# Optimization experiments

Hardware: AMD Instinct MI355X
Metric: run time of the kernel (lower is better)

The kernel has to match this reference:

```python
import jax, jax.numpy as jnp
import numpy as np

B = 8192      # graphs per batch
NPG = 40      # nodes per graph (= average_nodes, uniform here)
DEG = 16      # avg degree
IN = 64
HID = 32
OUT = 10
K1 = 20       # ceil(0.5*40)
K2 = 10       # ceil(0.5*20)
N = B * NPG
E = N * DEG
EPS = 1e-15


def _lin_params(k, fi, fo):
    kw, kb = jax.random.split(k)
    s = 1.0 / np.sqrt(fi)
    w = jax.random.uniform(kw, (fi, fo), jnp.float32, -s, s)
    b = jax.random.uniform(kb, (fo,), jnp.float32, -s, s)
    return w, b


def setup_inputs():
    key = jax.random.key(0)
    ks = jax.random.split(key, 14)
    x = jax.random.normal(ks[0], (N, IN), jnp.float32)
    # edges constrained within each graph (graphs are contiguous blocks of NPG nodes)
    g = jnp.repeat(jnp.arange(B, dtype=jnp.int32), NPG * DEG)
    src = g * NPG + jax.random.randint(ks[1], (E,), 0, NPG, dtype=jnp.int32)
    dst = g * NPG + jax.random.randint(ks[2], (E,), 0, NPG, dtype=jnp.int32)
    edge_index = jnp.stack([src, dst])
    batch = jnp.repeat(jnp.arange(B, dtype=jnp.int32), NPG)
    w_c1, b_c1 = _lin_params(ks[3], IN, HID)
    w_p1, b_p1 = _lin_params(ks[4], HID, K1)
    w2r, b2 = _lin_params(ks[5], HID, HID)
    w2o, _ = _lin_params(ks[6], HID, HID)
    w_p2, b_p2 = _lin_params(ks[7], HID, K2)
    w3r, b3 = _lin_params(ks[8], HID, HID)
    w3o, _ = _lin_params(ks[9], HID, HID)
    w_l1, b_l1 = _lin_params(ks[10], HID, HID)
    w_l2, b_l2 = _lin_params(ks[11], HID, OUT)
    return dict(x=x, edge_index=edge_index, batch=batch,
                w_c1=w_c1, b_c1=b_c1, w_p1=w_p1, b_p1=b_p1,
                w2r=w2r, b2=b2, w2o=w2o, w_p2=w_p2, b_p2=b_p2,
                w3r=w3r, b3=b3, w3o=w3o,
                w_l1=w_l1, b_l1=b_l1, w_l2=w_l2, b_l2=b_l2)


def _gcn_conv(x, edge_index, w, b):
    # PyG GCNConv: x' = D^-1/2 (A + I) D^-1/2 (X W) + b, unit edge weights
    h = x @ w
    row, col = edge_index
    deg = jnp.zeros((N,), h.dtype).at[col].add(1.0) + 1.0  # +1 self loop
    dinv = jax.lax.rsqrt(deg)
    msg = (dinv[row] * dinv[col])[:, None] * h[row]
    out = jnp.zeros_like(h).at[col].add(msg)
    out = out + (dinv * dinv)[:, None] * h  # self-loop contribution
    return out + b


def _dense_mincut_pool(x, adj, s, mask=None):
    # faithful to torch_geometric.nn.dense_mincut_pool
    s = jax.nn.softmax(s, axis=-1)
    if mask is not None:
        m = mask[..., None].astype(x.dtype)
        x = x * m
        s = s * m
    k = s.shape[-1]
    out = jnp.einsum('bnk,bnf->bkf', s, x)
    out_adj = jnp.einsum('bnk,bnm,bml->bkl', s, adj, s)
    mincut_num = jnp.trace(out_adj, axis1=1, axis2=2)
    d_flat = adj.sum(-1)                                   # [B, n]
    mincut_den = jnp.einsum('bnk,bn,bnk->b', s, d_flat, s)  # tr(S^T D S)
    mincut_loss = jnp.mean(-(mincut_num / mincut_den))
    ss = jnp.einsum('bnk,bnl->bkl', s, s)
    ss_norm = jnp.sqrt(jnp.sum(ss * ss, axis=(1, 2), keepdims=True))
    i_s = jnp.eye(k, dtype=x.dtype) / jnp.sqrt(jnp.asarray(k, x.dtype))
    ortho_loss = jnp.mean(jnp.sqrt(jnp.sum((ss / ss_norm - i_s) ** 2, axis=(1, 2))))
    # zero diagonal, then symmetric degree-normalize coarse adjacency
    eye = jnp.eye(k, dtype=x.dtype)
    out_adj = out_adj * (1.0 - eye)
    d = jnp.sqrt(out_adj.sum(-1))[:, None, :] + EPS        # [B,1,k]
    out_adj = out_adj / d / jnp.swapaxes(d, 1, 2)
    return out, out_adj, mincut_loss, ortho_loss


def _dense_graph_conv(x, adj, w_rel, b, w_root):
    # PyG DenseGraphConv (aggr='add'): lin_rel(A @ x) + lin_root(x); lin_root bias=False
    return (adj @ x) @ w_rel + b + x @ w_root


def reference(x, edge_index, batch, w_c1, b_c1, w_p1, b_p1, w2r, b2, w2o,
              w_p2, b_p2, w3r, b3, w3o, w_l1, b_l1, w_l2, b_l2):
    h = jax.nn.relu(_gcn_conv(x, edge_index, w_c1, b_c1))
    # to_dense_batch (uniform NPG nodes per graph, batch sorted)
    local = jnp.arange(N, dtype=jnp.int32) - batch * NPG
    xd = jnp.zeros((B, NPG, HID), h.dtype).at[batch, local].set(h)
    mask = jnp.ones((B, NPG), bool)
    # to_dense_adj (accumulates duplicate edges)
    row, col = edge_index
    g = batch[row]
    adj = jnp.zeros((B, NPG, NPG), h.dtype).at[g, row - g * NPG, col - g * NPG].add(1.0)
    s = xd @ w_p1 + b_p1
    xd, adj, mc1, o1 = _dense_mincut_pool(xd, adj, s, mask)
    xd = jax.nn.relu(_dense_graph_conv(xd, adj, w2r, b2, w2o))
    s = xd @ w_p2 + b_p2
    xd, adj, mc2, o2 = _dense_mincut_pool(xd, adj, s)
    xd = _dense_graph_conv(xd, adj, w3r, b3, w3o)
    pooled = xd.mean(axis=1)
    out = jax.nn.relu(pooled @ w_l1 + b_l1) @ w_l2 + b_l2
    return out, mc1 + mc2 + o1 + o2
```

## Files before the change

### kernel.cpp

```cpp
#include <hip/hip_runtime.h>

#define NT 256

constexpr int Bg   = 8192;
constexpr int NPG  = 40;
constexpr int EPG  = 640;
constexpr int IN_  = 64;
constexpr int HID  = 32;
constexpr int K1   = 20;
constexpr int K2   = 10;
constexpr int OUTC = 10;
constexpr int NE   = Bg * NPG * 16;
constexpr int SH   = 36;
constexpr float EPSF = 1e-15f;

#define FMA4(acc, a, b) do { \
    float _s = (a); \
    acc.x = fmaf(_s, (b).x, acc.x); \
    acc.y = fmaf(_s, (b).y, acc.y); \
    acc.z = fmaf(_s, (b).z, acc.z); \
    acc.w = fmaf(_s, (b).w, acc.w); } while (0)

__device__ __forceinline__ float wave_red(float v) {
#pragma unroll
    for (int off = 32; off > 0; off >>= 1) v += __shfl_down(v, off, 64);
    return v;
}

__global__ __launch_bounds__(NT, 4)
void mincut_fused(const float* __restrict__ x, const int* __restrict__ ei,
                  const float* __restrict__ w_c1, const float* __restrict__ b_c1,
                  const float* __restrict__ w_p1, const float* __restrict__ b_p1,
                  const float* __restrict__ w2r_, const float* __restrict__ b2_,
                  const float* __restrict__ w2o_,
                  const float* __restrict__ w_p2, const float* __restrict__ b_p2,
                  const float* __restrict__ w3r_, const float* __restrict__ b3_,
                  const float* __restrict__ w3o_,
                  const float* __restrict__ w_l1, const float* __restrict__ b_l1,
                  const float* __restrict__ w_l2, const float* __restrict__ b_l2,
                  float* __restrict__ out, float* __restrict__ wsg)
{
    __shared__ __align__(16) float sA_[NPG * NPG];
    __shared__ __align__(16) float bufH[NPG * SH];
    __shared__ __align__(16) float bufXd[NPG * SH];
    __shared__ __align__(16) float bufS[NPG * K1];
    __shared__ __align__(16) float bufAS[NPG * K1];
    __shared__ __align__(16) float sSS[K1 * K1];
    __shared__ __align__(16) float sdinv[NPG];
    __shared__ __align__(16) float srowsA[NPG];
    __shared__ __align__(16) float srowm[NPG];
    __shared__ __align__(16) float sden[NPG];
    __shared__ __align__(16) float sred1[2];
    __shared__ __align__(16) float sred2[2];
    __shared__ __align__(16) float sc[8];

    float* sA2  = sA_;
    float* sX2  = bufH;
    float* sW2r = bufH + 720;
    float* sW2o = bufAS;
    float* sS2  = bufS;
    float* sAS2 = bufS + 200;
    float* sA3  = bufS + 400;
    float* sSS2 = bufS + 500;
    float* sW3r = bufXd;
    float* sW3o = bufXd + 360;
    float* sX3  = bufXd + 720;
    float* sX4  = bufXd + 1080;

    const int g    = blockIdx.x;
    const int tid  = threadIdx.x;
    const int lane = tid & 63;
    const int wid  = tid >> 6;

    int er0, ec0, er1, ec1, er2 = -1, ec2 = 0;
    {
        const int eb = g * EPG, nb = g * NPG;
        const int* srcp = ei;
        const int* dstp = ei + NE;
        int e = eb + tid;
        er0 = srcp[e] - nb; ec0 = dstp[e] - nb;
        e += NT;
        er1 = srcp[e] - nb; ec1 = dstp[e] - nb;
        if (tid + 2 * NT < EPG) {
            e += NT;
            er2 = srcp[e] - nb; ec2 = dstp[e] - nb;
        }
    }
    for (int i = tid; i < NPG * NPG; i += NT) sA_[i] = 0.f;
    __syncthreads();

    atomicAdd(&sA_[er0 * NPG + ec0], 1.f);
    atomicAdd(&sA_[er1 * NPG + ec1], 1.f);
    if (er2 >= 0) atomicAdd(&sA_[er2 * NPG + ec2], 1.f);

    if (tid < 160) {
        int np = tid >> 3, fq = tid & 7;
        int n0 = 2 * np, n1 = n0 + 1;
        const float4* x0 = (const float4*)(x + (size_t)g * (NPG * IN_) + n0 * IN_);
        const float4* x1 = (const float4*)(x + (size_t)g * (NPG * IN_) + n1 * IN_);
        const float4* wg = (const float4*)w_c1;
        float4 acc0 = {0.f,0.f,0.f,0.f}, acc1 = {0.f,0.f,0.f,0.f};
#pragma unroll 4
        for (int kk = 0; kk < IN_ / 4; kk++) {
            float4 a0 = x0[kk], a1 = x1[kk];
            float4 w0 = wg[(4*kk+0)*8 + fq];
            float4 w1 = wg[(4*kk+1)*8 + fq];
            float4 w2 = wg[(4*kk+2)*8 + fq];
            float4 w3 = wg[(4*kk+3)*8 + fq];
            FMA4(acc0, a0.x, w0); FMA4(acc0, a0.y, w1);
            FMA4(acc0, a0.z, w2); FMA4(acc0, a0.w, w3);
            FMA4(acc1, a1.x, w0); FMA4(acc1, a1.y, w1);
            FMA4(acc1, a1.z, w2); FMA4(acc1, a1.w, w3);
        }
        ((float4*)(bufH + n0 * SH))[fq] = acc0;
        ((float4*)(bufH + n1 * SH))[fq] = acc1;
    }
    __syncthreads();

    if (tid < NPG) {
        float s = 0.f;
#pragma unroll
        for (int r = 0; r < NPG; r++) s += sA_[r * NPG + tid];
        sdinv[tid] = rsqrtf(s + 1.f);
    } else if (tid >= 64 && tid < 64 + NPG) {
        int n = tid - 64; float s = 0.f;
#pragma unroll
        for (int m = 0; m < NPG; m++) s += sA_[n * NPG + m];
        srowsA[n] = s;
    }
    __syncthreads();

    if (tid < 160) {
        int cp = tid >> 3, fq = tid & 7;
        int c0 = 2 * cp, c1 = c0 + 1;
        float4 acc0 = {0.f,0.f,0.f,0.f}, acc1 = {0.f,0.f,0.f,0.f};
#pragma unroll 8
        for (int r = 0; r < NPG; r++) {
            float2 a2 = *(const float2*)&sA_[r * NPG + c0];
            float dv = sdinv[r];
            float4 b = ((const float4*)(bufH + r * SH))[fq];
            FMA4(acc0, a2.x * dv, b);
            FMA4(acc1, a2.y * dv, b);
        }
        float4 bb = ((const float4*)b_c1)[fq];
        float4 h0 = ((const float4*)(bufH + c0 * SH))[fq];
        float4 h1 = ((const float4*)(bufH + c1 * SH))[fq];
        float d0 = sdinv[c0], d1 = sdinv[c1];
        float4 r0, r1;
        r0.x = fmaxf(fmaf(d0, fmaf(d0, h0.x, acc0.x), bb.x), 0.f);
        r0.y = fmaxf(fmaf(d0, fmaf(d0, h0.y, acc0.y), bb.y), 0.f);
        r0.z = fmaxf(fmaf(d0, fmaf(d0, h0.z, acc0.z), bb.z), 0.f);
        r0.w = fmaxf(fmaf(d0, fmaf(d0, h0.w, acc0.w), bb.w), 0.f);
        r1.x = fmaxf(fmaf(d1, fmaf(d1, h1.x, acc1.x), bb.x), 0.f);
        r1.y = fmaxf(fmaf(d1, fmaf(d1, h1.y, acc1.y), bb.y), 0.f);
        r1.z = fmaxf(fmaf(d1, fmaf(d1, h1.z, acc1.z), bb.z), 0.f);
        r1.w = fmaxf(fmaf(d1, fmaf(d1, h1.w, acc1.w), bb.w), 0.f);
        ((float4*)(bufXd + c0 * SH))[fq] = r0;
        ((float4*)(bufXd + c1 * SH))[fq] = r1;
    }
    __syncthreads();

    if (tid < 100) {
        int np = tid / 5, lq = tid - np * 5;
        int n0 = 2 * np, n1 = n0 + 1;
        const float4* wg = (const float4*)w_p1;
        float4 bb = ((const float4*)b_p1)[lq];
        float4 acc0 = bb, acc1 = bb;
#pragma unroll 8
        for (int k = 0; k < HID; k++) {
            float a0 = bufXd[n0 * SH + k];
            float a1 = bufXd[n1 * SH + k];
            float4 w = wg[k * 5 + lq];
            FMA4(acc0, a0, w);
            FMA4(acc1, a1, w);
        }
        ((float4*)(bufS + n0 * K1))[lq] = acc0;
        ((float4*)(bufS + n1 * K1))[lq] = acc1;
    }
    __syncthreads();

    if (tid < NPG) {
        float* row = bufS + tid * K1;
        float v[K1]; float m = -3.0e38f;
#pragma unroll
        for (int k = 0; k < K1; k++) { v[k] = row[k]; m = fmaxf(m, v[k]); }
        float ssum = 0.f;
#pragma unroll
        for (int k = 0; k < K1; k++) { v[k] = __expf(v[k] - m); ssum += v[k]; }
        float inv = 1.f / ssum;
#pragma unroll
        for (int k = 0; k < K1; k++) row[k] = v[k] * inv;
    }
    __syncthreads();

    if (tid < 100) {
        int np = tid / 5, lq = tid - np * 5;
        int n0 = 2 * np, n1 = n0 + 1;
        const float4* sb = (const float4*)bufS;
        float4 acc0 = {0.f,0.f,0.f,0.f}, acc1 = {0.f,0.f,0.f,0.f};
#pragma unroll
        for (int m4 = 0; m4 < NPG / 4; m4++) {
            float4 a0 = *(const float4*)&sA_[n0 * NPG + 4 * m4];
            float4 a1 = *(const float4*)&sA_[n1 * NPG + 4 * m4];
            float4 b0 = sb[(4*m4+0)*5 + lq];
            float4 b1 = sb[(4*m4+1)*5 + lq];
            float4 b2v = sb[(4*m4+2)*5 + lq];
            float4 b3v = sb[(4*m4+3)*5 + lq];
            FMA4(acc0, a0.x, b0); FMA4(acc0, a0.y, b1);
            FMA4(acc0, a0.z, b2v); FMA4(acc0, a0.w, b3v);
            FMA4(acc1, a1.x, b0); FMA4(acc1, a1.y, b1);
            FMA4(acc1, a1.z, b2v); FMA4(acc1, a1.w, b3v);
        }
        ((float4*)(bufAS + n0 * K1))[lq] = acc0;
        ((float4*)(bufAS + n1 * K1))[lq] = acc1;
    } else if (tid < 150) {
        int oo = tid - 100;
        int kp = oo / 5, lq = oo - kp * 5;
        int k0 = 2 * kp, k1 = k0 + 1;
        float4 acc0 = {0.f,0.f,0.f,0.f}, acc1 = {0.f,0.f,0.f,0.f};
#pragma unroll 8
        for (int n = 0; n < NPG; n++) {
            float2 s2v = *(const float2*)&bufS[n * K1 + k0];
            float4 b = ((const float4*)(bufS + n * K1))[lq];
            FMA4(acc0, s2v.x, b);
            FMA4(acc1, s2v.y, b);
        }
        ((float4*)(sSS + k0 * K1))[lq] = acc0;
        ((float4*)(sSS + k1 * K1))[lq] = acc1;
    }
    __syncthreads();

    if (tid < 50) {
        int kp = tid / 5, lq = tid - kp * 5;
        int k0 = 2 * kp, k1 = k0 + 1;
        float4 acc0 = {0.f,0.f,0.f,0.f}, acc1 = {0.f,0.f,0.f,0.f};
#pragma unroll 8
        for (int n = 0; n < NPG; n++) {
            float2 s2v = *(const float2*)&bufS[n * K1 + k0];
            float4 b = ((const float4*)(bufAS + n * K1))[lq];
            FMA4(acc0, s2v.x, b);
            FMA4(acc1, s2v.y, b);
        }
        ((float4*)(sA2 + k0 * K1))[lq] = acc0;
        ((float4*)(sA2 + k1 * K1))[lq] = acc1;
    } else if (tid < 130) {
        int oo = tid - 50;
        int kp = oo >> 3, fq = oo & 7;
        int k0 = 2 * kp, k1 = k0 + 1;
        float4 acc0 = {0.f,0.f,0.f,0.f}, acc1 = {0.f,0.f,0.f,0.f};
#pragma unroll 8
        for (int n = 0; n < NPG; n++) {
            float2 s2v = *(const float2*)&bufS[n * K1 + k0];
            float4 b = ((const float4*)(bufXd + n * SH))[fq];
            FMA4(acc0, s2v.x, b);
            FMA4(acc1, s2v.y, b);
        }
        ((float4*)(sX2 + k0 * SH))[fq] = acc0;
        ((float4*)(sX2 + k1 * SH))[fq] = acc1;
    } else if (tid < 170) {
        int n = tid - 130;
        float s2 = 0.f;
#pragma unroll
        for (int k = 0; k < K1; k++) { float v = bufS[n * K1 + k]; s2 = fmaf(v, v, s2); }
        sden[n] = srowsA[n] * s2;
    } else if (wid == 3) {
        float v = 0.f;
        for (int i = lane; i < K1 * K1; i += 64) { float t = sSS[i]; v = fmaf(t, t, v); }
        v = wave_red(v); if (lane == 0) sc[2] = v;
    }
    __syncthreads();

    if (wid < 2) {
        float rn = 1.f / sqrtf(sc[2]);
        const float isk = 0.22360679774997896f;
        float p = 0.f;
        for (int o = tid; o < K1 * K1; o += 128) {
            int k = o / K1, l = o - k * K1;
            float v = sSS[o] * rn - ((k == l) ? isk : 0.f);
            p = fmaf(v, v, p);
        }
        p = wave_red(p);
        if (lane == 0) sred1[wid] = p;
    } else if (wid == 2) {
        float v = (lane < K1) ? sA2[lane * (K1 + 1)] : 0.f;
        v = wave_red(v); if (lane == 0) sc[0] = v;
        if (lane < K1) {
            float s = 0.f;
#pragma unroll
            for (int l = 0; l < K1; l++) s += sA2[lane * K1 + l];
            s -= sA2[lane * (K1 + 1)];
            srowm[lane] = 1.f / (sqrtf(s) + EPSF);
        }
    } else {
        float v = (lane < NPG) ? sden[lane] : 0.f;
        v = wave_red(v); if (lane == 0) sc[1] = v;
    }
    for (int o = tid; o < 320; o += NT) {
        bool first = (o < 160);
        int oo = first ? o : o - 160;
        int n = oo >> 3, fq = oo & 7;
        const float4* wg = (const float4*)(first ? w2r_ : w2o_);
        float4 acc = {0.f,0.f,0.f,0.f};
#pragma unroll 8
        for (int k = 0; k < HID; k++) {
            float a = sX2[n * SH + k];
            FMA4(acc, a, wg[k * 8 + fq]);
        }
        if (first) ((float4*)(sW2r + n * SH))[fq] = acc;
        else       ((float4*)(sW2o + n * SH))[fq] = acc;
    }
    __syncthreads();

    if (tid < 80) {
        int kp = tid >> 3, fq = tid & 7;
        int k0 = 2 * kp, k1 = k0 + 1;
        float4 acc0 = {0.f,0.f,0.f,0.f}, acc1 = {0.f,0.f,0.f,0.f};
#pragma unroll
        for (int l = 0; l < K1; l++) {
            float rl = srowm[l];
            float a0 = (l == k0) ? 0.f : sA2[k0 * K1 + l];
            float a1 = (l == k1) ? 0.f : sA2[k1 * K1 + l];
            float4 w = ((const float4*)(sW2r + l * SH))[fq];
            FMA4(acc0, a0 * rl, w);
            FMA4(acc1, a1 * rl, w);
        }
        float4 bb = ((const float4*)b2_)[fq];
        float4 o0 = ((const float4*)(sW2o + k0 * SH))[fq];
        float4 o1 = ((const float4*)(sW2o + k1 * SH))[fq];
        float rk0 = srowm[k0], rk1 = srowm[k1];
        float4 r0, r1;
        r0.x = fmaxf(fmaf(rk0, acc0.x, o0.x + bb.x), 0.f);
        r0.y = fmaxf(fmaf(rk0, acc0.y, o0.y + bb.y), 0.f);
        r0.z = fmaxf(fmaf(rk0, acc0.z, o0.z + bb.z), 0.f);
        r0.w = fmaxf(fmaf(rk0, acc0.w, o0.w + bb.w), 0.f);
        r1.x = fmaxf(fmaf(rk1, acc1.x, o1.x + bb.x), 0.f);
        r1.y = fmaxf(fmaf(rk1, acc1.y, o1.y + bb.y), 0.f);
        r1.z = fmaxf(fmaf(rk1, acc1.z, o1.z + bb.z), 0.f);
        r1.w = fmaxf(fmaf(rk1, acc1.w, o1.w + bb.w), 0.f);
        ((float4*)(sX2 + k0 * SH))[fq] = r0;
        ((float4*)(sX2 + k1 * SH))[fq] = r1;
    }
    __syncthreads();

    if (tid < K1 * K2) {
        int n = tid / K2, q = tid - n * K2;
        float acc = b_p2[q];
#pragma unroll 8
        for (int j = 0; j < HID; j++) acc = fmaf(sX2[n * SH + j], w_p2[j * K2 + q], acc);
        sS2[tid] = acc;
    }
    __syncthreads();

    if (tid < K1) {
        float* row = sS2 + tid * K2;
        float v[K2]; float m = -3.0e38f;
#pragma unroll
        for (int q = 0; q < K2; q++) { v[q] = row[q]; m = fmaxf(m, v[q]); }
        float ssum = 0.f;
#pragma unroll
        for (int q = 0; q < K2; q++) { v[q] = __expf(v[q] - m); ssum += v[q]; }
        float inv = 1.f / ssum;
#pragma unroll
        for (int q = 0; q < K2; q++) row[q] = v[q] * inv;
    }
    __syncthreads();

    for (int o = tid; o < 400; o += NT) {
        if (o < 200) {
            int n = o / K2, l = o - n * K2;
            float acc = 0.f;
#pragma unroll
            for (int m = 0; m < K1; m++) {
                float a = (m == n) ? 0.f : sA2[n * K1 + m];
                acc = fmaf(a * srowm[m], sS2[m * K2 + l], acc);
            }
            sAS2[n * K2 + l] = acc * srowm[n];
        } else if (o < 300) {
            int oo = o - 200; int k = oo / K2, l = oo - k * K2;
            float acc = 0.f;
#pragma unroll
            for (int n = 0; n < K1; n++) acc = fmaf(sS2[n * K2 + k], sS2[n * K2 + l], acc);
            sSS2[k * K2 + l] = acc;
        } else if (o < 380) {
            int oo = o - 300; int k = oo >> 3, fq = oo & 7;
            float4 acc = {0.f, 0.f, 0.f, 0.f};
#pragma unroll
            for (int n = 0; n < K1; n++) {
                float a = sS2[n * K2 + k];
                float4 b = ((const float4*)(sX2 + n * SH))[fq];
                FMA4(acc, a, b);
            }
            ((float4*)(sX3 + k * SH))[fq] = acc;
        } else {
            int n = o - 380;
            float da = 0.f, s2 = 0.f;
#pragma unroll
            for (int l = 0; l < K1; l++) {
                float a = (l == n) ? 0.f : sA2[n * K1 + l];
                da = fmaf(a, srowm[l], da);
            }
            da *= srowm[n];
#pragma unroll
            for (int q = 0; q < K2; q++) { float v = sS2[n * K2 + q]; s2 = fmaf(v, v, s2); }
            sden[n] = da * s2;
        }
    }
    __syncthreads();

    if (tid < K2 * K2) {
        int k = tid / K2, l = tid - k * K2;
        float acc = 0.f;
#pragma unroll
        for (int n = 0; n < K1; n++) acc = fmaf(sS2[n * K2 + k], sAS2[n * K2 + l], acc);
        sA3[tid] = acc;
    } else if (wid == 2) {
        float v = (lane < K1) ? sden[lane] : 0.f;
        v = wave_red(v); if (lane == 0) sc[5] = v;
    } else if (wid == 3) {
        float v = 0.f;
        for (int i = lane; i < K2 * K2; i += 64) { float t = sSS2[i]; v = fmaf(t, t, v); }
        v = wave_red(v); if (lane == 0) sc[6] = v;
    }
    __syncthreads();

    if (wid == 0) {
        float rn = 1.f / sqrtf(sc[6]);
        const float isk = 0.31622776601683794f;
        float p = 0.f;
        for (int i = lane; i < K2 * K2; i += 64) {
            int k = i / K2, l = i - k * K2;
            float v = sSS2[i] * rn - ((k == l) ? isk : 0.f);
            p = fmaf(v, v, p);
        }
        p = wave_red(p);
        if (lane == 0) sred2[0] = p;
    } else if (wid == 1) {
        float v = (lane < K2) ? sA3[lane * (K2 + 1)] : 0.f;
        v = wave_red(v); if (lane == 0) sc[4] = v;
        if (lane < K2) {
            float s = 0.f;
#pragma unroll
            for (int l = 0; l < K2; l++) s += sA3[lane * K2 + l];
            s -= sA3[lane * (K2 + 1)];
            srowm[lane] = 1.f / (sqrtf(s) + EPSF);
        }
    }
    __syncthreads();

    if (tid < 160) {
        bool first = (tid < 80);
        int oo = first ? tid : tid - 80;
        int n = oo >> 3, fq = oo & 7;
        const float4* wg = (const float4*)(first ? w3r_ : w3o_);
        float4 acc = {0.f,0.f,0.f,0.f};
#pragma unroll 8
        for (int k = 0; k < HID; k++) {
            float a = sX3[n * SH + k];
            FMA4(acc, a, wg[k * 8 + fq]);
        }
        if (first) ((float4*)(sW3r + n * SH))[fq] = acc;
        else       ((float4*)(sW3o + n * SH))[fq] = acc;
    } else if (tid == 200) {
        float o1 = sqrtf(sred1[0] + sred1[1]);
        float o2 = sqrtf(sred2[0]);
        wsg[g] = -(sc[0] / sc[1]) + o1 - (sc[4] / sc[5]) + o2;
    }
    __syncthreads();

    if (tid < 40) {
        int kp = tid >> 3, fq = tid & 7;
        int k0 = 2 * kp, k1 = k0 + 1;
        float4 acc0 = {0.f,0.f,0.f,0.f}, acc1 = {0.f,0.f,0.f,0.f};
#pragma unroll
        for (int l = 0; l < K2; l++) {
            float rl = srowm[l];
            float a0 = (l == k0) ? 0.f : sA3[k0 * K2 + l];
            float a1 = (l == k1) ? 0.f : sA3[k1 * K2 + l];
            float4 w = ((const float4*)(sW3r + l * SH))[fq];
            FMA4(acc0, a0 * rl, w);
            FMA4(acc1, a1 * rl, w);
        }
        float4 bb = ((const float4*)b3_)[fq];
        float4 o0 = ((const float4*)(sW3o + k0 * SH))[fq];
        float4 o1 = ((const float4*)(sW3o + k1 * SH))[fq];
        float rk0 = srowm[k0], rk1 = srowm[k1];
        float4 r0, r1;
        r0.x = fmaf(rk0, acc0.x, o0.x + bb.x);
        r0.y = fmaf(rk0, acc0.y, o0.y + bb.y);
        r0.z = fmaf(rk0, acc0.z, o0.z + bb.z);
        r0.w = fmaf(rk0, acc0.w, o0.w + bb.w);
        r1.x = fmaf(rk1, acc1.x, o1.x + bb.x);
        r1.y = fmaf(rk1, acc1.y, o1.y + bb.y);
        r1.z = fmaf(rk1, acc1.z, o1.z + bb.z);
        r1.w = fmaf(rk1, acc1.w, o1.w + bb.w);
        ((float4*)(sX4 + k0 * SH))[fq] = r0;
        ((float4*)(sX4 + k1 * SH))[fq] = r1;
    }
    __syncthreads();

    if (wid == 0) {
        int f = lane & 31;
        float pool = 0.f;
#pragma unroll
        for (int n = 0; n < K2; n++) pool += sX4[n * SH + f];
        pool *= (1.f / K2);
        float acc = b_l1[f];
#pragma unroll
        for (int j = 0; j < HID; j++)
            acc = fmaf(__shfl(pool, j, 64), w_l1[j * HID + f], acc);
        float t1 = fmaxf(acc, 0.f);
        int o = (lane < OUTC) ? lane : 0;
        float acc2 = b_l2[o];
#pragma unroll
        for (int j = 0; j < HID; j++)
            acc2 = fmaf(__shfl(t1, j, 64), w_l2[j * OUTC + o], acc2);
        if (lane < OUTC) out[(size_t)g * OUTC + lane] = acc2;
    }
}

__global__ void loss_reduce(const float* __restrict__ wsg, float* __restrict__ out)
{
    __shared__ float sred[4];
    int tid = threadIdx.x;
    float s = 0.f;
    for (int i = tid; i < Bg; i += NT) s += wsg[i];
    s = wave_red(s);
    if ((tid & 63) == 0) sred[tid >> 6] = s;
    __syncthreads();
    if (tid == 0) out[(size_t)Bg * OUTC] = (sred[0] + sred[1] + sred[2] + sred[3]) * (1.f / Bg);
}

extern "C" void kernel_launch(void* const* d_in, const int* in_sizes, int n_in,
                              void* d_out, int out_size, void* d_ws, size_t ws_size,
                              hipStream_t stream)
{
    const float* x    = (const float*)d_in[0];
    const int*   ei   = (const int*)  d_in[1];
    const float* w_c1 = (const float*)d_in[3];
    const float* b_c1 = (const float*)d_in[4];
    const float* w_p1 = (const float*)d_in[5];
    const float* b_p1 = (const float*)d_in[6];
    const float* w2r  = (const float*)d_in[7];
    const float* b2   = (const float*)d_in[8];
    const float* w2o  = (const float*)d_in[9];
    const float* w_p2 = (const float*)d_in[10];
    const float* b_p2 = (const float*)d_in[11];
    const float* w3r  = (const float*)d_in[12];
    const float* b3   = (const float*)d_in[13];
    const float* w3o  = (const float*)d_in[14];
    const float* w_l1 = (const float*)d_in[15];
    const float* b_l1 = (const float*)d_in[16];
    const float* w_l2 = (const float*)d_in[17];
    const float* b_l2 = (const float*)d_in[18];
    float* out = (float*)d_out;
    float* wsg = (float*)d_ws;

    hipLaunchKernelGGL(mincut_fused, dim3(Bg), dim3(NT), 0, stream,
                       x, ei, w_c1, b_c1, w_p1, b_p1, w2r, b2, w2o,
                       w_p2, b_p2, w3r, b3, w3o, w_l1, b_l1, w_l2, b_l2,
                       out, wsg);
    hipLaunchKernelGGL(loss_reduce, dim3(1), dim3(NT), 0, stream, wsg, out);
}
```

Before: 286.1 us.

## Stage node features in LDS, use closed-form orthogonality loss, reorder conv2 matmuls

Node features for each graph are first loaded cooperatively into a padded shared-memory tile, so the first linear layer reads them from LDS instead of issuing strided global float4 loads per thread pair. The orthogonality loss is computed in closed form, sqrt(2 - 2*trace/(||SS||*sqrt(k))), which removes a reduction pass and a barrier at both pooling levels. The stage-2 graph conv now aggregates first and applies the weight afterwards, and per-row normalisation is moved into stages that already exist. Shared-memory buffers are reorganised into new aliased regions, which brings a risk of aliasing mistakes and a changed occupancy footprint.

```diff
diff --git a/kernel.cpp b/kernel.cpp
--- a/kernel.cpp
+++ b/kernel.cpp
@@ -11,6 +11,7 @@
 constexpr int K2   = 10;
 constexpr int OUTC = 10;
 constexpr int NE   = Bg * NPG * 16;
+constexpr int SX   = 68;
 constexpr int SH   = 36;
 constexpr float EPSF = 1e-15f;
 
@@ -40,32 +41,28 @@
                   const float* __restrict__ w_l2, const float* __restrict__ b_l2,
                   float* __restrict__ out, float* __restrict__ wsg)
 {
-    __shared__ __align__(16) float sA_[NPG * NPG];
-    __shared__ __align__(16) float bufH[NPG * SH];
-    __shared__ __align__(16) float bufXd[NPG * SH];
-    __shared__ __align__(16) float bufS[NPG * K1];
-    __shared__ __align__(16) float bufAS[NPG * K1];
-    __shared__ __align__(16) float sSS[K1 * K1];
+    __shared__ __align__(16) float sA[NPG * NPG];
+    __shared__ __align__(16) float sXbuf[NPG * SX];
+    __shared__ __align__(16) float sH[NPG * SH];
+    __shared__ __align__(16) float sXd[NPG * SH];
     __shared__ __align__(16) float sdinv[NPG];
     __shared__ __align__(16) float srowsA[NPG];
     __shared__ __align__(16) float srowm[NPG];
     __shared__ __align__(16) float sden[NPG];
-    __shared__ __align__(16) float sred1[2];
-    __shared__ __align__(16) float sred2[2];
     __shared__ __align__(16) float sc[8];
 
-    float* sA2  = sA_;
-    float* sX2  = bufH;
-    float* sW2r = bufH + 720;
-    float* sW2o = bufAS;
-    float* sS2  = bufS;
-    float* sAS2 = bufS + 200;
-    float* sA3  = bufS + 400;
-    float* sSS2 = bufS + 500;
-    float* sW3r = bufXd;
-    float* sW3o = bufXd + 360;
-    float* sX3  = bufXd + 720;
-    float* sX4  = bufXd + 1080;
+    float* sA2  = sA;
+    float* sS   = sXbuf;
+    float* sAS  = sXbuf + 800;
+    float* sSS  = sXbuf + 1600;
+    float* sX2  = sH;
+    float* sS2  = sH + 720;
+    float* sX3  = sH + 920;
+    float* sA3  = sH + 1280;
+    float* sXw2o= sXd;
+    float* sW3r = sXd;
+    float* sW3o = sXd + 360;
+    float* sX4  = sH;
 
     const int g    = blockIdx.x;
     const int tid  = threadIdx.x;
@@ -75,34 +72,39 @@
     int er0, ec0, er1, ec1, er2 = -1, ec2 = 0;
     {
         const int eb = g * EPG, nb = g * NPG;
-        const int* srcp = ei;
-        const int* dstp = ei + NE;
         int e = eb + tid;
-        er0 = srcp[e] - nb; ec0 = dstp[e] - nb;
+        er0 = ei[e] - nb; ec0 = ei[NE + e] - nb;
         e += NT;
-        er1 = srcp[e] - nb; ec1 = dstp[e] - nb;
+        er1 = ei[e] - nb; ec1 = ei[NE + e] - nb;
         if (tid + 2 * NT < EPG) {
             e += NT;
-            er2 = srcp[e] - nb; ec2 = dstp[e] - nb;
-        }
-    }
-    for (int i = tid; i < NPG * NPG; i += NT) sA_[i] = 0.f;
-    __syncthreads();
-
-    atomicAdd(&sA_[er0 * NPG + ec0], 1.f);
-    atomicAdd(&sA_[er1 * NPG + ec1], 1.f);
-    if (er2 >= 0) atomicAdd(&sA_[er2 * NPG + ec2], 1.f);
+            er2 = ei[e] - nb; ec2 = ei[NE + e] - nb;
+        }
+    }
+    for (int i = tid; i < NPG * NPG; i += NT) sA[i] = 0.f;
+    {
+        const float4* xg = (const float4*)(x + (size_t)g * (NPG * IN_));
+        for (int i = tid; i < NPG * (IN_ / 4); i += NT) {
+            int n = i >> 4, k = i & 15;
+            ((float4*)(sXbuf + n * SX))[k] = xg[i];
+        }
+    }
+    __syncthreads();
+
+    atomicAdd(&sA[er0 * NPG + ec0], 1.f);
+    atomicAdd(&sA[er1 * NPG + ec1], 1.f);
+    if (er2 >= 0) atomicAdd(&sA[er2 * NPG + ec2], 1.f);
 
     if (tid < 160) {
         int np = tid >> 3, fq = tid & 7;
         int n0 = 2 * np, n1 = n0 + 1;
-        const float4* x0 = (const float4*)(x + (size_t)g * (NPG * IN_) + n0 * IN_);
-        const float4* x1 = (const float4*)(x + (size_t)g * (NPG * IN_) + n1 * IN_);
-        const float4* wg = (const float4*)w_c1;
+        const float4* a0p = (const float4*)(sXbuf + n0 * SX);
+        const float4* a1p = (const float4*)(sXbuf + n1 * SX);
+        const float4* wg  = (const float4*)w_c1;
         float4 acc0 = {0.f,0.f,0.f,0.f}, acc1 = {0.f,0.f,0.f,0.f};
 #pragma unroll 4
         for (int kk = 0; kk < IN_ / 4; kk++) {
-            float4 a0 = x0[kk], a1 = x1[kk];
+            float4 a0 = a0p[kk], a1 = a1p[kk];
             float4 w0 = wg[(4*kk+0)*8 + fq];
             float4 w1 = wg[(4*kk+1)*8 + fq];
             float4 w2 = wg[(4*kk+2)*8 + fq];
@@ -112,20 +114,20 @@
             FMA4(acc1, a1.x, w0); FMA4(acc1, a1.y, w1);
             FMA4(acc1, a1.z, w2); FMA4(acc1, a1.w, w3);
         }
-        ((float4*)(bufH + n0 * SH))[fq] = acc0;
-        ((float4*)(bufH + n1 * SH))[fq] = acc1;
+        ((float4*)(sH + n0 * SH))[fq] = acc0;
+        ((float4*)(sH + n1 * SH))[fq] = acc1;
     }
     __syncthreads();
 
     if (tid < NPG) {
         float s = 0.f;
 #pragma unroll
-        for (int r = 0; r < NPG; r++) s += sA_[r * NPG + tid];
+        for (int r = 0; r < NPG; r++) s += sA[r * NPG + tid];
         sdinv[tid] = rsqrtf(s + 1.f);
     } else if (tid >= 64 && tid < 64 + NPG) {
         int n = tid - 64; float s = 0.f;
 #pragma unroll
-        for (int m = 0; m < NPG; m++) s += sA_[n * NPG + m];
+        for (int m = 0; m < NPG; m++) s += sA[n * NPG + m];
         srowsA[n] = s;
     }
     __syncthreads();
@@ -136,15 +138,15 @@
         float4 acc0 = {0.f,0.f,0.f,0.f}, acc1 = {0.f,0.f,0.f,0.f};
 #pragma unroll 8
         for (int r = 0; r < NPG; r++) {
-            float2 a2 = *(const float2*)&sA_[r * NPG + c0];
+            float2 a2 = *(const float2*)&sA[r * NPG + c0];
             float dv = sdinv[r];
-            float4 b = ((const float4*)(bufH + r * SH))[fq];
-            FMA4(acc0, a2.x * dv, b);
-            FMA4(acc1, a2.y * dv, b);
+            float4 bv = ((const float4*)(sH + r * SH))[fq];
+            FMA4(acc0, a2.x * dv, bv);
+            FMA4(acc1, a2.y * dv, bv);
         }
         float4 bb = ((const float4*)b_c1)[fq];
-        float4 h0 = ((const float4*)(bufH + c0 * SH))[fq];
-        float4 h1 = ((const float4*)(bufH + c1 * SH))[fq];
+        float4 h0 = ((const float4*)(sH + c0 * SH))[fq];
+        float4 h1 = ((const float4*)(sH + c1 * SH))[fq];
         float d0 = sdinv[c0], d1 = sdinv[c1];
         float4 r0, r1;
         r0.x = fmaxf(fmaf(d0, fmaf(d0, h0.x, acc0.x), bb.x), 0.f);
@@ -155,8 +157,8 @@
         r1.y = fmaxf(fmaf(d1, fmaf(d1, h1.y, acc1.y), bb.y), 0.f);
         r1.z = fmaxf(fmaf(d1, fmaf(d1, h1.z, acc1.z), bb.z), 0.f);
         r1.w = fmaxf(fmaf(d1, fmaf(d1, h1.w, acc1.w), bb.w), 0.f);
-        ((float4*)(bufXd + c0 * SH))[fq] = r0;
-        ((float4*)(bufXd + c1 * SH))[fq] = r1;
+        ((float4*)(sXd + c0 * SH))[fq] = r0;
+        ((float4*)(sXd + c1 * SH))[fq] = r1;
     }
     __syncthreads();
 
@@ -168,19 +170,18 @@
         float4 acc0 = bb, acc1 = bb;
 #pragma unroll 8
         for (int k = 0; k < HID; k++) {
-            float a0 = bufXd[n0 * SH + k];
-            float a1 = bufXd[n1 * SH + k];
+            float a0 = sXd[n0 * SH + k];
+            float a1 = sXd[n1 * SH + k];
             float4 w = wg[k * 5 + lq];
-            FMA4(acc0, a0, w);
-            FMA4(acc1, a1, w);
-        }
-        ((float4*)(bufS + n0 * K1))[lq] = acc0;
-        ((float4*)(bufS + n1 * K1))[lq] = acc1;
+            FMA4(acc0, a0, w); FMA4(acc1, a1, w);
+        }
+        ((float4*)(sS + n0 * K1))[lq] = acc0;
+        ((float4*)(sS + n1 * K1))[lq] = acc1;
     }
     __syncthreads();
 
     if (tid < NPG) {
-        float* row = bufS + tid * K1;
+        float* row = sS + tid * K1;
         float v[K1]; float m = -3.0e38f;
 #pragma unroll
         for (int k = 0; k < K1; k++) { v[k] = row[k]; m = fmaxf(m, v[k]); }
@@ -196,12 +197,12 @@
     if (tid < 100) {
         int np = tid / 5, lq = tid - np * 5;
         int n0 = 2 * np, n1 = n0 + 1;
-        const float4* sb = (const float4*)bufS;
+        const float4* sb = (const float4*)sS;
         float4 acc0 = {0.f,0.f,0.f,0.f}, acc1 = {0.f,0.f,0.f,0.f};
 #pragma unroll
         for (int m4 = 0; m4 < NPG / 4; m4++) {
-            float4 a0 = *(const float4*)&sA_[n0 * NPG + 4 * m4];
-            float4 a1 = *(const float4*)&sA_[n1 * NPG + 4 * m4];
+            float4 a0 = *(const float4*)&sA[n0 * NPG + 4 * m4];
+            float4 a1 = *(const float4*)&sA[n1 * NPG + 4 * m4];
             float4 b0 = sb[(4*m4+0)*5 + lq];
             float4 b1 = sb[(4*m4+1)*5 + lq];
             float4 b2v = sb[(4*m4+2)*5 + lq];
@@ -211,8 +212,8 @@
             FMA4(acc1, a1.x, b0); FMA4(acc1, a1.y, b1);
             FMA4(acc1, a1.z, b2v); FMA4(acc1, a1.w, b3v);
         }
-        ((float4*)(bufAS + n0 * K1))[lq] = acc0;
-        ((float4*)(bufAS + n1 * K1))[lq] = acc1;
+        ((float4*)(sAS + n0 * K1))[lq] = acc0;
+        ((float4*)(sAS + n1 * K1))[lq] = acc1;
     } else if (tid < 150) {
         int oo = tid - 100;
         int kp = oo / 5, lq = oo - kp * 5;
@@ -220,10 +221,9 @@
         float4 acc0 = {0.f,0.f,0.f,0.f}, acc1 = {0.f,0.f,0.f,0.f};
 #pragma unroll 8
         for (int n = 0; n < NPG; n++) {
-            float2 s2v = *(const float2*)&bufS[n * K1 + k0];
-            float4 b = ((const float4*)(bufS + n * K1))[lq];
-            FMA4(acc0, s2v.x, b);
-            FMA4(acc1, s2v.y, b);
+            float2 s2v = *(const float2*)&sS[n * K1 + k0];
+            float4 bv = ((const float4*)(sS + n * K1))[lq];
+            FMA4(acc0, s2v.x, bv); FMA4(acc1, s2v.y, bv);
         }
         ((float4*)(sSS + k0 * K1))[lq] = acc0;
         ((float4*)(sSS + k1 * K1))[lq] = acc1;
@@ -236,10 +236,9 @@
         float4 acc0 = {0.f,0.f,0.f,0.f}, acc1 = {0.f,0.f,0.f,0.f};
 #pragma unroll 8
         for (int n = 0; n < NPG; n++) {
-            float2 s2v = *(const float2*)&bufS[n * K1 + k0];
-            float4 b = ((const float4*)(bufAS + n * K1))[lq];
-            FMA4(acc0, s2v.x, b);
-            FMA4(acc1, s2v.y, b);
+            float2 s2v = *(const float2*)&sS[n * K1 + k0];
+            float4 bv = ((const float4*)(sAS + n * K1))[lq];
+            FMA4(acc0, s2v.x, bv); FMA4(acc1, s2v.y, bv);
         }
         ((float4*)(sA2 + k0 * K1))[lq] = acc0;
         ((float4*)(sA2 + k1 * K1))[lq] = acc1;
@@ -250,10 +249,9 @@
         float4 acc0 = {0.f,0.f,0.f,0.f}, acc1 = {0.f,0.f,0.f,0.f};
 #pragma unroll 8
         for (int n = 0; n < NPG; n++) {
-            float2 s2v = *(const float2*)&bufS[n * K1 + k0];
-            float4 b = ((const float4*)(bufXd + n * SH))[fq];
-            FMA4(acc0, s2v.x, b);
-            FMA4(acc1, s2v.y, b);
+            float2 s2v = *(const float2*)&sS[n * K1 + k0];
+            float4 bv = ((const float4*)(sXd + n * SH))[fq];
+            FMA4(acc0, s2v.x, bv); FMA4(acc1, s2v.y, bv);
         }
         ((float4*)(sX2 + k0 * SH))[fq] = acc0;
         ((float4*)(sX2 + k1 * SH))[fq] = acc1;
@@ -261,84 +259,82 @@
         int n = tid - 130;
         float s2 = 0.f;
 #pragma unroll
-        for (int k = 0; k < K1; k++) { float v = bufS[n * K1 + k]; s2 = fmaf(v, v, s2); }
+        for (int k = 0; k < K1; k++) { float v = sS[n * K1 + k]; s2 = fmaf(v, v, s2); }
         sden[n] = srowsA[n] * s2;
-    } else if (wid == 3) {
+    }
+    __syncthreads();
+
+    if (wid == 0) {
+        float f = 0.f, tr = 0.f;
+        for (int i = lane; i < K1 * K1; i += 64) {
+            float t = sSS[i];
+            f = fmaf(t, t, f);
+            if (i % (K1 + 1) == 0) tr += t;
+        }
+        f = wave_red(f); tr = wave_red(tr);
+        if (lane == 0)
+            sc[2] = sqrtf(fmaxf(2.f - 2.f * tr / (sqrtf(f) * 4.47213595499958f), 0.f));
+    } else if (wid == 1) {
         float v = 0.f;
-        for (int i = lane; i < K1 * K1; i += 64) { float t = sSS[i]; v = fmaf(t, t, v); }
-        v = wave_red(v); if (lane == 0) sc[2] = v;
-    }
-    __syncthreads();
-
-    if (wid < 2) {
-        float rn = 1.f / sqrtf(sc[2]);
-        const float isk = 0.22360679774997896f;
-        float p = 0.f;
-        for (int o = tid; o < K1 * K1; o += 128) {
-            int k = o / K1, l = o - k * K1;
-            float v = sSS[o] * rn - ((k == l) ? isk : 0.f);
-            p = fmaf(v, v, p);
-        }
-        p = wave_red(p);
-        if (lane == 0) sred1[wid] = p;
-    } else if (wid == 2) {
-        float v = (lane < K1) ? sA2[lane * (K1 + 1)] : 0.f;
-        v = wave_red(v); if (lane == 0) sc[0] = v;
         if (lane < K1) {
             float s = 0.f;
 #pragma unroll
             for (int l = 0; l < K1; l++) s += sA2[lane * K1 + l];
-            s -= sA2[lane * (K1 + 1)];
-            srowm[lane] = 1.f / (sqrtf(s) + EPSF);
-        }
-    } else {
+            float d = sA2[lane * (K1 + 1)];
+            srowm[lane] = 1.f / (sqrtf(s - d) + EPSF);
+            v = d;
+        }
+        v = wave_red(v);
+        if (lane == 0) sc[0] = v;
+    } else if (wid == 2) {
         float v = (lane < NPG) ? sden[lane] : 0.f;
-        v = wave_red(v); if (lane == 0) sc[1] = v;
-    }
-    for (int o = tid; o < 320; o += NT) {
-        bool first = (o < 160);
-        int oo = first ? o : o - 160;
-        int n = oo >> 3, fq = oo & 7;
-        const float4* wg = (const float4*)(first ? w2r_ : w2o_);
+        v = wave_red(v);
+        if (lane == 0) sc[1] = v;
+    }
+    if (tid < 160) {
+        int n = tid >> 3, fq = tid & 7;
+        const float4* wg = (const float4*)w2o_;
         float4 acc = {0.f,0.f,0.f,0.f};
 #pragma unroll 8
         for (int k = 0; k < HID; k++) {
             float a = sX2[n * SH + k];
             FMA4(acc, a, wg[k * 8 + fq]);
         }
-        if (first) ((float4*)(sW2r + n * SH))[fq] = acc;
-        else       ((float4*)(sW2o + n * SH))[fq] = acc;
-    }
-    __syncthreads();
-
-    if (tid < 80) {
-        int kp = tid >> 3, fq = tid & 7;
-        int k0 = 2 * kp, k1 = k0 + 1;
-        float4 acc0 = {0.f,0.f,0.f,0.f}, acc1 = {0.f,0.f,0.f,0.f};
+        ((float4*)(sXw2o + n * SH))[fq] = acc;
+    }
+    __syncthreads();
+
+    if (tid < 160) {
+        int k = tid >> 3, fq = tid & 7;
+        float4 acc = {0.f,0.f,0.f,0.f};
 #pragma unroll
         for (int l = 0; l < K1; l++) {
-            float rl = srowm[l];
-            float a0 = (l == k0) ? 0.f : sA2[k0 * K1 + l];
-            float a1 = (l == k1) ? 0.f : sA2[k1 * K1 + l];
-            float4 w = ((const float4*)(sW2r + l * SH))[fq];
-            FMA4(acc0, a0 * rl, w);
-            FMA4(acc1, a1 * rl, w);
-        }
+            float a = (l == k) ? 0.f : sA2[k * K1 + l];
+            float4 bv = ((const float4*)(sX2 + l * SH))[fq];
+            FMA4(acc, a * srowm[l], bv);
+        }
+        float rk = srowm[k];
+        acc.x *= rk; acc.y *= rk; acc.z *= rk; acc.w *= rk;
+        ((float4*)(sAS + k * SH))[fq] = acc;
+    }
+    __syncthreads();
+
+    if (tid < 160) {
+        int k = tid >> 3, fq = tid & 7;
+        const float4* wg = (const float4*)w2r_;
         float4 bb = ((const float4*)b2_)[fq];
-        float4 o0 = ((const float4*)(sW2o + k0 * SH))[fq];
-        float4 o1 = ((const float4*)(sW2o + k1 * SH))[fq];
-        float rk0 = srowm[k0], rk1 = srowm[k1];
-        float4 r0, r1;
-        r0.x = fmaxf(fmaf(rk0, acc0.x, o0.x + bb.x), 0.f);
-        r0.y = fmaxf(fmaf(rk0, acc0.y, o0.y + bb.y), 0.f);
-        r0.z = fmaxf(fmaf(rk0, acc0.z, o0.z + bb.z), 0.f);
-        r0.w = fmaxf(fmaf(rk0, acc0.w, o0.w + bb.w), 0.f);
-        r1.x = fmaxf(fmaf(rk1, acc1.x, o1.x + bb.x), 0.f);
-        r1.y = fmaxf(fmaf(rk1, acc1.y, o1.y + bb.y), 0.f);
-        r1.z = fmaxf(fmaf(rk1, acc1.z, o1.z + bb.z), 0.f);
-        r1.w = fmaxf(fmaf(rk1, acc1.w, o1.w + bb.w), 0.f);
-        ((float4*)(sX2 + k0 * SH))[fq] = r0;
-        ((float4*)(sX2 + k1 * SH))[fq] = r1;
+        float4 oo = ((const float4*)(sXw2o + k * SH))[fq];
+        float4 acc;
+        acc.x = bb.x + oo.x; acc.y = bb.y + oo.y;
+        acc.z = bb.z + oo.z; acc.w = bb.w + oo.w;
+#pragma unroll 8
+        for (int j = 0; j < HID; j++) {
+            float a = sAS[k * SH + j];
+            FMA4(acc, a, wg[j * 8 + fq]);
+        }
+        acc.x = fmaxf(acc.x, 0.f); acc.y = fmaxf(acc.y, 0.f);
+        acc.z = fmaxf(acc.z, 0.f); acc.w = fmaxf(acc.w, 0.f);
+        ((float4*)(sX2 + k * SH))[fq] = acc;
     }
     __syncthreads();
 
@@ -374,21 +370,21 @@
                 float a = (m == n) ? 0.f : sA2[n * K1 + m];
                 acc = fmaf(a * srowm[m], sS2[m * K2 + l], acc);
             }
-            sAS2[n * K2 + l] = acc * srowm[n];
+            sAS[n * K2 + l] = acc * srowm[n];
         } else if (o < 300) {
             int oo = o - 200; int k = oo / K2, l = oo - k * K2;
             float acc = 0.f;
 #pragma unroll
             for (int n = 0; n < K1; n++) acc = fmaf(sS2[n * K2 + k], sS2[n * K2 + l], acc);
-            sSS2[k * K2 + l] = acc;
+            sSS[oo] = acc;
         } else if (o < 380) {
             int oo = o - 300; int k = oo >> 3, fq = oo & 7;
-            float4 acc = {0.f, 0.f, 0.f, 0.f};
+            float4 acc = {0.f,0.f,0.f,0.f};
 #pragma unroll
             for (int n = 0; n < K1; n++) {
                 float a = sS2[n * K2 + k];
-                float4 b = ((const float4*)(sX2 + n * SH))[fq];
-                FMA4(acc, a, b);
+                float4 bv = ((const float4*)(sX2 + n * SH))[fq];
+                FMA4(acc, a, bv);
             }
             ((float4*)(sX3 + k * SH))[fq] = acc;
         } else {
@@ -411,39 +407,22 @@
         int k = tid / K2, l = tid - k * K2;
         float acc = 0.f;
 #pragma unroll
-        for (int n = 0; n < K1; n++) acc = fmaf(sS2[n * K2 + k], sAS2[n * K2 + l], acc);
+        for (int n = 0; n < K1; n++) acc = fmaf(sS2[n * K2 + k], sAS[n * K2 + l], acc);
         sA3[tid] = acc;
     } else if (wid == 2) {
         float v = (lane < K1) ? sden[lane] : 0.f;
-        v = wave_red(v); if (lane == 0) sc[5] = v;
+        v = wave_red(v);
+        if (lane == 0) sc[5] = v;
     } else if (wid == 3) {
-        float v = 0.f;
-        for (int i = lane; i < K2 * K2; i += 64) { float t = sSS2[i]; v = fmaf(t, t, v); }
-        v = wave_red(v); if (lane == 0) sc[6] = v;
-    }
-    __syncthreads();
-
-    if (wid == 0) {
-        float rn = 1.f / sqrtf(sc[6]);
-        const float isk = 0.31622776601683794f;
-        float p = 0.f;
+        float f = 0.f, tr = 0.f;
         for (int i = lane; i < K2 * K2; i += 64) {
-            int k = i / K2, l = i - k * K2;
-            float v = sSS2[i] * rn - ((k == l) ? isk : 0.f);
-            p = fmaf(v, v, p);
-        }
-        p = wave_red(p);
-        if (lane == 0) sred2[0] = p;
-    } else if (wid == 1) {
-        float v = (lane < K2) ? sA3[lane * (K2 + 1)] : 0.f;
-        v = wave_red(v); if (lane == 0) sc[4] = v;
-        if (lane < K2) {
-            float s = 0.f;
-#pragma unroll
-            for (int l = 0; l < K2; l++) s += sA3[lane * K2 + l];
-            s -= sA3[lane * (K2 + 1)];
-            srowm[lane] = 1.f / (sqrtf(s) + EPSF);
-        }
+            float t = sSS[i];
+            f = fmaf(t, t, f);
+            if (i % (K2 + 1) == 0) tr += t;
+        }
+        f = wave_red(f); tr = wave_red(tr);
+        if (lane == 0)
+            sc[6] = sqrtf(fmaxf(2.f - 2.f * tr / (sqrtf(f) * 3.1622776601683795f), 0.f));
     }
     __syncthreads();
 
@@ -460,41 +439,39 @@
         }
         if (first) ((float4*)(sW3r + n * SH))[fq] = acc;
         else       ((float4*)(sW3o + n * SH))[fq] = acc;
+    } else if (tid >= 160 && tid < 160 + K2) {
+        int l = tid - 160;
+        float s = 0.f;
+#pragma unroll
+        for (int m = 0; m < K2; m++) s += sA3[l * K2 + m];
+        s -= sA3[l * (K2 + 1)];
+        srowm[l] = 1.f / (sqrtf(s) + EPSF);
     } else if (tid == 200) {
-        float o1 = sqrtf(sred1[0] + sred1[1]);
-        float o2 = sqrtf(sred2[0]);
-        wsg[g] = -(sc[0] / sc[1]) + o1 - (sc[4] / sc[5]) + o2;
-    }
-    __syncthreads();
-
-    if (tid < 40) {
-        int kp = tid >> 3, fq = tid & 7;
-        int k0 = 2 * kp, k1 = k0 + 1;
-        float4 acc0 = {0.f,0.f,0.f,0.f}, acc1 = {0.f,0.f,0.f,0.f};
+        float num2 = 0.f;
+#pragma unroll
+        for (int k = 0; k < K2; k++) num2 += sA3[k * (K2 + 1)];
+        wsg[g] = -(sc[0] / sc[1]) + sc[2] - num2 / sc[5] + sc[6];
+    }
+    __syncthreads();
+
+    if (tid < 80) {
+        int k = tid >> 3, fq = tid & 7;
+        float4 acc = {0.f,0.f,0.f,0.f};
 #pragma unroll
         for (int l = 0; l < K2; l++) {
-            float rl = srowm[l];
-            float a0 = (l == k0) ? 0.f : sA3[k0 * K2 + l];
-            float a1 = (l == k1) ? 0.f : sA3[k1 * K2 + l];
+            float a = (l == k) ? 0.f : sA3[k * K2 + l];
             float4 w = ((const float4*)(sW3r + l * SH))[fq];
-            FMA4(acc0, a0 * rl, w);
-            FMA4(acc1, a1 * rl, w);
+            FMA4(acc, a * srowm[l], w);
         }
         float4 bb = ((const float4*)b3_)[fq];
-        float4 o0 = ((const float4*)(sW3o + k0 * SH))[fq];
-        float4 o1 = ((const float4*)(sW3o + k1 * SH))[fq];
-        float rk0 = srowm[k0], rk1 = srowm[k1];
-        float4 r0, r1;
-        r0.x = fmaf(rk0, acc0.x, o0.x + bb.x);
-        r0.y = fmaf(rk0, acc0.y, o0.y + bb.y);
-        r0.z = fmaf(rk0, acc0.z, o0.z + bb.z);
-        r0.w = fmaf(rk0, acc0.w, o0.w + bb.w);
-        r1.x = fmaf(rk1, acc1.x, o1.x + bb.x);
-        r1.y = fmaf(rk1, acc1.y, o1.y + bb.y);
-        r1.z = fmaf(rk1, acc1.z, o1.z + bb.z);
-        r1.w = fmaf(rk1, acc1.w, o1.w + bb.w);
-        ((float4*)(sX4 + k0 * SH))[fq] = r0;
-        ((float4*)(sX4 + k1 * SH))[fq] = r1;
+        float4 oo = ((const float4*)(sW3o + k * SH))[fq];
+        float rk = srowm[k];
+        float4 r;
+        r.x = fmaf(rk, acc.x, oo.x + bb.x);
+        r.y = fmaf(rk, acc.y, oo.y + bb.y);
+        r.z = fmaf(rk, acc.z, oo.z + bb.z);
+        r.w = fmaf(rk, acc.w, oo.w + bb.w);
+        ((float4*)(sX4 + k * SH))[fq] = r;
     }
     __syncthreads();
 
```

After: 258.3 us. -9.7%, faster.
